# Kernel optimization log

Measured on AMD Instinct MI355X. Metric: run time of the kernel, lower is better.

The kernel has to match this reference:

```python
import jax, jax.numpy as jnp
import numpy as np

B, P, D, N = 32, 3, 300, 2048

def setup_inputs() -> dict:
    key = jax.random.key(0)
    k1, k2 = jax.random.split(key)
    input_data1 = jax.random.normal(k1, (B, P, D, N), dtype=jnp.float32)
    input_data2 = jax.random.normal(k2, (B, P, D, N), dtype=jnp.float32)
    return {"input_data1": input_data1, "input_data2": input_data2}

def reference(input_data1, input_data2):
    # Horizontal comparison: permute(0,1,3,2) -> vectors of length D at each
    # (batch, pool, position); compute cos, l2, l1 distance per vector pair.
    x = jnp.transpose(input_data1, (0, 1, 3, 2))  # [B,P,N,D]
    y = jnp.transpose(input_data2, (0, 1, 3, 2))  # [B,P,N,D]
    dot = jnp.sum(x * y, axis=-1)
    xn = jnp.sqrt(jnp.sum(x * x, axis=-1))
    yn = jnp.sqrt(jnp.sum(y * y, axis=-1))
    cos = dot / (xn * yn)                      # [B,P,N]
    d = x - y
    l2 = jnp.sqrt(jnp.sum(d * d, axis=-1))     # [B,P,N]
    l1 = jnp.sum(jnp.abs(d), axis=-1)          # [B,P,N]  (sqrt((x-y)^2).sum())
    out = jnp.stack([cos, l2, l1], axis=-1)    # [B,P,N,3]
    b = out.shape[0]
    return out.reshape(b, -1, out.shape[-1])   # [B, P*N, 3]
```

## Files before the change

kernel.cpp:

```cpp
#include <hip/hip_runtime.h>
#include <math.h>


constexpr int kB = 32;
constexpr int kP = 3;
constexpr int kD = 300;
constexpr int kN = 2048;
constexpr int kSeg = 4;
constexpr int kDSeg = kD / kSeg;

__device__ inline void reduce4(float4& v) {
    v.x += __shfl_down(v.x, 32); v.y += __shfl_down(v.y, 32);
    v.z += __shfl_down(v.z, 32); v.w += __shfl_down(v.w, 32);
    v.x += __shfl_down(v.x, 16); v.y += __shfl_down(v.y, 16);
    v.z += __shfl_down(v.z, 16); v.w += __shfl_down(v.w, 16);
}

__global__ __launch_bounds__(256) void sim_measure_kernel(
    const float* __restrict__ x,
    const float* __restrict__ y,
    float* __restrict__ out)
{
    const int tid  = blockIdx.x * 256 + threadIdx.x;
    const int lane = tid & 63;
    const int wave = tid >> 6;

    const int q = lane & 15;
    const int s = lane >> 4;

    const int bp = wave >> 5;
    const int n0 = (wave & 31) << 6;

    const size_t base = ((size_t)bp * kD + (size_t)s * kDSeg) * kN + (size_t)(n0 + q * 4);
    const float4* __restrict__ xp = (const float4*)(x + base);
    const float4* __restrict__ yp = (const float4*)(y + base);
    constexpr int kStride4 = kN / 4;

    float4 dot = {0.f, 0.f, 0.f, 0.f};
    float4 xx  = {0.f, 0.f, 0.f, 0.f};
    float4 yy  = {0.f, 0.f, 0.f, 0.f};
    float4 l2s = {0.f, 0.f, 0.f, 0.f};
    float4 l1  = {0.f, 0.f, 0.f, 0.f};

    #pragma unroll 5
    for (int d = 0; d < kDSeg; ++d) {
        const float4 xv = xp[(size_t)d * kStride4];
        const float4 yv = yp[(size_t)d * kStride4];

        dot.x = fmaf(xv.x, yv.x, dot.x); dot.y = fmaf(xv.y, yv.y, dot.y);
        dot.z = fmaf(xv.z, yv.z, dot.z); dot.w = fmaf(xv.w, yv.w, dot.w);
        xx.x  = fmaf(xv.x, xv.x, xx.x);  xx.y  = fmaf(xv.y, xv.y, xx.y);
        xx.z  = fmaf(xv.z, xv.z, xx.z);  xx.w  = fmaf(xv.w, xv.w, xx.w);
        yy.x  = fmaf(yv.x, yv.x, yy.x);  yy.y  = fmaf(yv.y, yv.y, yy.y);
        yy.z  = fmaf(yv.z, yv.z, yy.z);  yy.w  = fmaf(yv.w, yv.w, yy.w);
        const float dx = xv.x - yv.x, dy = xv.y - yv.y,
                    dz = xv.z - yv.z, dw = xv.w - yv.w;
        l2s.x = fmaf(dx, dx, l2s.x); l2s.y = fmaf(dy, dy, l2s.y);
        l2s.z = fmaf(dz, dz, l2s.z); l2s.w = fmaf(dw, dw, l2s.w);
        l1.x += fabsf(dx); l1.y += fabsf(dy);
        l1.z += fabsf(dz); l1.w += fabsf(dw);
    }

    reduce4(dot); reduce4(xx); reduce4(yy); reduce4(l2s); reduce4(l1);

    if (s == 0) {
        float4 o0, o1, o2;
        const float c0 = dot.x / (sqrtf(xx.x) * sqrtf(yy.x));
        const float c1 = dot.y / (sqrtf(xx.y) * sqrtf(yy.y));
        const float c2 = dot.z / (sqrtf(xx.z) * sqrtf(yy.z));
        const float c3 = dot.w / (sqrtf(xx.w) * sqrtf(yy.w));
        const float e0 = sqrtf(l2s.x), e1 = sqrtf(l2s.y),
                    e2 = sqrtf(l2s.z), e3 = sqrtf(l2s.w);

        o0.x = c0;   o0.y = e0;   o0.z = l1.x; o0.w = c1;
        o1.x = e1;   o1.y = l1.y; o1.z = c2;   o1.w = e2;
        o2.x = l1.z; o2.y = c3;   o2.z = e3;   o2.w = l1.w;

        float4* op = (float4*)(out + ((size_t)bp * kN + (size_t)(n0 + q * 4)) * 3);
        op[0] = o0; op[1] = o1; op[2] = o2;
    }
}

extern "C" void kernel_launch(void* const* d_in, const int* in_sizes, int n_in,
                              void* d_out, int out_size, void* d_ws, size_t ws_size,
                              hipStream_t stream)
{
    const float* x = (const float*)d_in[0];
    const float* y = (const float*)d_in[1];
    float* out = (float*)d_out;

    const int total = kB * kP * kN;
    const int block = 256;
    const int grid  = total / block;

    sim_measure_kernel<<<grid, block, 0, stream>>>(x, y, out);
}
```

Baseline: 453.3 us.

## Split D reduction across three waves per block with LDS combine

Each block now handles one 64-column tile using three waves, each reducing a third of the D dimension. Partial sums are combined through shared memory after a block barrier. This raises the number of waves and memory requests in flight per output tile and shortens each wave's serial load chain, aiming for better latency hiding on a bandwidth-bound reduction. In exchange it adds an LDS round-trip, a __syncthreads, and leaves two of three waves idle during the final write.

```diff
diff --git a/kernel.cpp b/kernel.cpp
--- a/kernel.cpp
+++ b/kernel.cpp
@@ -6,8 +6,9 @@
 constexpr int kP = 3;
 constexpr int kD = 300;
 constexpr int kN = 2048;
+constexpr int kWaves = 3;
 constexpr int kSeg = 4;
-constexpr int kDSeg = kD / kSeg;
+constexpr int kRows = kD / (kWaves * kSeg);
 
 __device__ inline void reduce4(float4& v) {
     v.x += __shfl_down(v.x, 32); v.y += __shfl_down(v.y, 32);
@@ -16,22 +17,22 @@
     v.z += __shfl_down(v.z, 16); v.w += __shfl_down(v.w, 16);
 }
 
-__global__ __launch_bounds__(256) void sim_measure_kernel(
+__global__ __launch_bounds__(192) void sim_measure_kernel(
     const float* __restrict__ x,
     const float* __restrict__ y,
     float* __restrict__ out)
 {
-    const int tid  = blockIdx.x * 256 + threadIdx.x;
-    const int lane = tid & 63;
-    const int wave = tid >> 6;
-
+    const int lane = threadIdx.x & 63;
+    const int ww   = threadIdx.x >> 6;
     const int q = lane & 15;
     const int s = lane >> 4;
 
-    const int bp = wave >> 5;
-    const int n0 = (wave & 31) << 6;
+    const int bp = blockIdx.x >> 5;
+    const int n0 = (blockIdx.x & 31) << 6;
 
-    const size_t base = ((size_t)bp * kD + (size_t)s * kDSeg) * kN + (size_t)(n0 + q * 4);
+    const int seg = ww * kSeg + s;
+    const size_t base = ((size_t)bp * kD + (size_t)seg * kRows) * kN
+                      + (size_t)(n0 + q * 4);
     const float4* __restrict__ xp = (const float4*)(x + base);
     const float4* __restrict__ yp = (const float4*)(y + base);
     constexpr int kStride4 = kN / 4;
@@ -43,7 +44,7 @@
     float4 l1  = {0.f, 0.f, 0.f, 0.f};
 
     #pragma unroll 5
-    for (int d = 0; d < kDSeg; ++d) {
+    for (int d = 0; d < kRows; ++d) {
         const float4 xv = xp[(size_t)d * kStride4];
         const float4 yv = yp[(size_t)d * kStride4];
 
@@ -63,7 +64,31 @@
 
     reduce4(dot); reduce4(xx); reduce4(yy); reduce4(l2s); reduce4(l1);
 
-    if (s == 0) {
+    __shared__ float4 lds[kWaves - 1][16][5];
+    if (ww > 0 && s == 0) {
+        lds[ww - 1][q][0] = dot;
+        lds[ww - 1][q][1] = xx;
+        lds[ww - 1][q][2] = yy;
+        lds[ww - 1][q][3] = l2s;
+        lds[ww - 1][q][4] = l1;
+    }
+    __syncthreads();
+
+    if (ww == 0 && s == 0) {
+        #pragma unroll
+        for (int w = 0; w < kWaves - 1; ++w) {
+            const float4 a = lds[w][q][0];
+            const float4 b = lds[w][q][1];
+            const float4 c = lds[w][q][2];
+            const float4 e = lds[w][q][3];
+            const float4 f = lds[w][q][4];
+            dot.x += a.x; dot.y += a.y; dot.z += a.z; dot.w += a.w;
+            xx.x  += b.x; xx.y  += b.y; xx.z  += b.z; xx.w  += b.w;
+            yy.x  += c.x; yy.y  += c.y; yy.z  += c.z; yy.w  += c.w;
+            l2s.x += e.x; l2s.y += e.y; l2s.z += e.z; l2s.w += e.w;
+            l1.x  += f.x; l1.y  += f.y; l1.z  += f.z; l1.w  += f.w;
+        }
+
         float4 o0, o1, o2;
         const float c0 = dot.x / (sqrtf(xx.x) * sqrtf(yy.x));
         const float c1 = dot.y / (sqrtf(xx.y) * sqrtf(yy.y));
@@ -89,9 +114,8 @@
     const float* y = (const float*)d_in[1];
     float* out = (float*)d_out;
 
-    const int total = kB * kP * kN;
-    const int block = 256;
-    const int grid  = total / block;
+    const int grid  = kB * kP * (kN / 64);
+    const int block = 64 * kWaves;
 
     sim_measure_kernel<<<grid, block, 0, stream>>>(x, y, out);
 }
```

Result: slower. 462.8 us (+2.1%).
